# Optimization experiments

Measured on AMD Instinct MI355X. Metric: run time of the kernel, lower is better.

The kernel has to match this reference:

```python
import math
import jax, jax.numpy as jnp
import numpy as np

HEADS = 16
DIM_HEAD = 64
BSZ = 16        # block_size
EPS = 1e-8


def _flip_every_two(t):
    # t: (B, nblk, z, d) -> flip adjacent pairs along nblk
    B, nblk = t.shape[0], t.shape[1]
    t = t.reshape(B, nblk // 2, 2, *t.shape[2:])
    t = jnp.flip(t, axis=2)
    return t.reshape(B, nblk, *t.shape[3:])


def setup_inputs() -> dict:
    key = jax.random.key(0)
    k1, k2, k3 = jax.random.split(key, 3)
    b, n, dim = 4, 8192, 1024
    inner = HEADS * DIM_HEAD
    x = jax.random.normal(k1, (b, n, dim), dtype=jnp.float32)
    w_qkv = jax.random.normal(k2, (dim, inner * 3), dtype=jnp.float32) * 0.02
    w_out = jax.random.normal(k3, (inner, dim), dtype=jnp.float32) * 0.02
    b_out = jnp.zeros((dim,), dtype=jnp.float32)
    return {"x": x, "w_qkv": w_qkv, "w_out": w_out, "b_out": b_out}


def _hattention(x, w_qkv, w_out, b_out):
    b, n, dim = x.shape  # n assumed power of 2 -> no padding needed
    scale = DIM_HEAD ** -0.5

    qkv = x @ w_qkv                                   # (b, n, 3*inner)
    q, k, v = jnp.split(qkv, 3, axis=-1)

    def to_heads(t):
        return t.reshape(b, n, HEADS, DIM_HEAD).transpose(0, 2, 1, 3).reshape(b * HEADS, n, DIM_HEAD)

    q, k, v = map(to_heads, (q, k, v))
    q = q * scale

    num_levels = int(math.log2(n // BSZ)) - 1

    # build coarsened pyramid: q,k averaged over pairs, v summed
    qkvs = [(q, k, v)]
    for _ in range(num_levels):
        B, m, d = q.shape
        q = q.reshape(B, m // 2, 2, d).mean(axis=2)
        k = k.reshape(B, m // 2, 2, d).mean(axis=2)
        v = v.reshape(B, m // 2, 2, d).sum(axis=2)
        qkvs.append((q, k, v))

    def to_blocks(t):
        return t.reshape(t.shape[0], -1, BSZ, DIM_HEAD)

    Ys = []
    L = len(qkvs)
    for ind, (ql, kl, vl) in enumerate(reversed(qkvs)):
        is_last = ind == L - 1
        qb, kb, vb = map(to_blocks, (ql, kl, vl))
        if not is_last:
            kb = _flip_every_two(kb)
            vb = _flip_every_two(vb)
        # block-local unnormalized softmax attention
        S = jnp.einsum('bnid,bnjd->bnij', qb, kb)
        S = S - jnp.max(S, axis=-1, keepdims=True)
        A = jnp.exp(S)
        y = jnp.einsum('bnij,bnjd->bnid', A, vb)
        Asum = A.sum(axis=-1)
        Ys.append((y.reshape(y.shape[0], -1, DIM_HEAD),
                   Asum.reshape(Asum.shape[0], -1)))

    # combine coarse-to-fine by upsampling (repeat by 2) and summing
    Y, A = Ys[0]
    for Yl, Al in Ys[1:]:
        Y = jnp.repeat(Y, 2, axis=1) + Yl
        A = jnp.repeat(A, 2, axis=1) + Al

    out = Y / (A + EPS)[..., None]                    # (b*h, n, d)
    out = out.reshape(b, HEADS, n, DIM_HEAD).transpose(0, 2, 1, 3).reshape(b, n, HEADS * DIM_HEAD)
    return out @ w_out + b_out


def reference(x, w_qkv, w_out, b_out):
    return _hattention(x, w_qkv, w_out, b_out)
```

## Files before the change

### kernel.cpp

```cpp
#include <hip/hip_runtime.h>
#include <hip/hip_bf16.h>

typedef __bf16 bf16_t;
typedef bf16_t bf16x8 __attribute__((ext_vector_type(8)));
typedef float f32x4 __attribute__((ext_vector_type(4)));

#define PROWS 16352

__device__ __forceinline__ void gl_lds16(const bf16_t* g, bf16_t* l) {
  __builtin_amdgcn_global_load_lds(
      (const __attribute__((address_space(1))) void*)g,
      (__attribute__((address_space(3))) void*)l,
      16, 0, 0);
}

__device__ __forceinline__ void load8f(const bf16_t* p, float* f) {
  bf16x8 v = *(const bf16x8*)p;
#pragma unroll
  for (int e = 0; e < 8; ++e) f[e] = (float)v[e];
}
__device__ __forceinline__ void store8f(bf16_t* p, const float* f) {
  bf16x8 v;
#pragma unroll
  for (int e = 0; e < 8; ++e) v[e] = (bf16_t)f[e];
  *(bf16x8*)p = v;
}

__global__ __launch_bounds__(256) void cvt_f32_to_bf16(const float* __restrict__ in,
                                                       bf16_t* __restrict__ o) {
  size_t gid = (size_t)blockIdx.x * 256 + threadIdx.x;
  const float4* p = (const float4*)in + gid * 2;
  float4 a = p[0], b = p[1];
  bf16x8 v;
  v[0] = (bf16_t)a.x; v[1] = (bf16_t)a.y; v[2] = (bf16_t)a.z; v[3] = (bf16_t)a.w;
  v[4] = (bf16_t)b.x; v[5] = (bf16_t)b.y; v[6] = (bf16_t)b.z; v[7] = (bf16_t)b.w;
  *(bf16x8*)(o + gid * 8) = v;
}

__global__ __launch_bounds__(256) void transpose_to_bf16(const float* __restrict__ w,
                                                         bf16_t* __restrict__ wT,
                                                         int K, int N) {
  __shared__ float t[32][33];
  int bx = blockIdx.x, by = blockIdx.y;
  int tx = threadIdx.x & 31, ty = threadIdx.x >> 5;
#pragma unroll
  for (int r = ty; r < 32; r += 8)
    t[r][tx] = w[(size_t)(by * 32 + r) * N + bx * 32 + tx];
  __syncthreads();
#pragma unroll
  for (int r = ty; r < 32; r += 8)
    wT[(size_t)(bx * 32 + r) * K + by * 32 + tx] = (bf16_t)t[tx][r];
}

template <int EPI>
__global__ __launch_bounds__(512, 2) void gemm256(const bf16_t* __restrict__ A,
                                                  const bf16_t* __restrict__ Bt,
                                                  float* __restrict__ Cp,
                                                  const float* __restrict__ bias,
                                                  bf16_t* __restrict__ Pq,
                                                  bf16_t* __restrict__ Pk,
                                                  bf16_t* __restrict__ Pv,
                                                  int K, int ldc, int nTilesN) {
  __shared__ __align__(16) bf16_t As[2 * 256 * 64];
  __shared__ __align__(16) bf16_t Bs[2 * 256 * 64];
  const int tid = threadIdx.x;
  const int w = tid >> 6, lane = tid & 63;

  int mt, ntile;
  if (EPI == 0) {
    const int x = blockIdx.x & 7;
    const int c = blockIdx.x >> 3;
    mt = (x & 3) * 32 + c / 6;
    ntile = (x >> 2) * 6 + c % 6;
  } else {
    int nwg = gridDim.x;
    int chunk = nwg >> 3;
    int wgid = (blockIdx.x & 7) * chunk + (blockIdx.x >> 3);
    mt = wgid / nTilesN; ntile = wgid % nTilesN;
  }
  const int bm = mt * 256, bn = ntile * 256;

  const int wr = w >> 2, wc = w & 3;
  const int lr = lane & 15, lg = lane >> 4;
  const int sw = lr & 7;
  const int nt = K >> 6;

  f32x4 acc[8][4] = {};

  auto stageHalf = [&](const bf16_t* __restrict__ G, int rbase, int kt, int ld,
                       bf16_t* lbuf, int h) {
#pragma unroll
    for (int j = 0; j < 2; ++j) {
      int b = j * 8 + w;
      int r3 = lane >> 3;
      int k8 = (lane & 7) ^ r3;
      gl_lds16(G + (size_t)(rbase + h * 128 + b * 8 + r3) * ld + kt + k8 * 8,
               lbuf + h * 8192 + b * 512);
    }
  };

  stageHalf(Bt, bn, 0, K, Bs, 0); stageHalf(Bt, bn, 0, K, Bs, 1);
  stageHalf(A, bm, 0, K, As, 0);  stageHalf(A, bm, 0, K, As, 1);
  if (nt > 1) {
    stageHalf(Bt, bn, 64, K, Bs + 16384, 0); stageHalf(Bt, bn, 64, K, Bs + 16384, 1);
    stageHalf(A, bm, 64, K, As + 16384, 0);  stageHalf(A, bm, 64, K, As + 16384, 1);
    asm volatile("s_waitcnt vmcnt(8)" ::: "memory");
  } else {
    asm volatile("s_waitcnt vmcnt(0)" ::: "memory");
  }
  __syncthreads();

  for (int t = 0; t < nt; ++t) {
    const int c = t & 1;
    bf16_t* Abuf = As + c * 16384;
    bf16_t* Bbuf = Bs + c * 16384;
    const bool pf = (t + 2) < nt;
    const int kt2 = (t + 2) << 6;
    bf16x8 bfrag[4][2];

#pragma unroll
    for (int p = 0; p < 4; ++p) {
      bf16x8 afrag[2][2];
#pragma unroll
      for (int fi = 0; fi < 2; ++fi)
#pragma unroll
        for (int kk = 0; kk < 2; ++kk)
          afrag[fi][kk] = *(const bf16x8*)&Abuf[(wr * 128 + p * 32 + fi * 16 + lr) * 64 +
                                                (((kk * 4 + lg) ^ sw) * 8)];
      if (p == 0) {
#pragma unroll
        for (int fj = 0; fj < 4; ++fj)
#pragma unroll
          for (int kk = 0; kk < 2; ++kk)
            bfrag[fj][kk] = *(const bf16x8*)&Bbuf[(wc * 64 + fj * 16 + lr) * 64 +
                                                  (((kk * 4 + lg) ^ sw) * 8)];
      }
      if (pf) {
        if (p == 1) stageHalf(Bt, bn, kt2, K, Bbuf, 0);
        if (p == 2) stageHalf(Bt, bn, kt2, K, Bbuf, 1);
        if (p == 3) { stageHalf(A, bm, kt2, K, Abuf, 0); stageHalf(A, bm, kt2, K, Abuf, 1); }
      }
      __builtin_amdgcn_s_barrier();
      asm volatile("s_waitcnt lgkmcnt(0)" ::: "memory");
      __builtin_amdgcn_sched_barrier(0);
      __builtin_amdgcn_s_setprio(1);
#pragma unroll
      for (int kk = 0; kk < 2; ++kk)
#pragma unroll
        for (int fi = 0; fi < 2; ++fi)
#pragma unroll
          for (int fj = 0; fj < 4; ++fj)
            acc[p * 2 + fi][fj] = __builtin_amdgcn_mfma_f32_16x16x32_bf16(
                afrag[fi][kk], bfrag[fj][kk], acc[p * 2 + fi][fj], 0, 0, 0);
      __builtin_amdgcn_s_setprio(0);
      if (p == 3) {
        if (pf) asm volatile("s_waitcnt vmcnt(8)" ::: "memory");
        else    asm volatile("s_waitcnt vmcnt(0)" ::: "memory");
      }
      __builtin_amdgcn_s_barrier();
    }
  }

  if (EPI == 1) {
    float bv[4];
#pragma unroll
    for (int fj = 0; fj < 4; ++fj) bv[fj] = bias[bn + wc * 64 + fj * 16 + lr];
#pragma unroll
    for (int fi = 0; fi < 8; ++fi)
#pragma unroll
      for (int fj = 0; fj < 4; ++fj)
#pragma unroll
        for (int r = 0; r < 4; ++r) {
          int row = bm + wr * 128 + fi * 16 + lg * 4 + r;
          int col = bn + wc * 64 + fj * 16 + lr;
          Cp[(size_t)row * ldc + col] = acc[fi][fj][r] + bv[fj];
        }
  } else {
    const int tns = bn >> 10;
    const int h = ((bn & 1023) >> 6) + wc;
    const int hgRow = (bm >> 13) << 4;
    const int trow0 = (bm & 8191) + wr * 128;
    bf16_t* Pt = (tns == 0) ? Pq : (tns == 1 ? Pk : Pv);
    const float scl = (tns == 0) ? 0.125f : 1.f;
    bf16_t* lds = (w < 4) ? (As + w * 4608) : (Bs + (w - 4) * 4608);
    const size_t gbase = ((size_t)(hgRow + h) * PROWS + trow0) * 64;
#pragma unroll
    for (int half = 0; half < 2; ++half) {
#pragma unroll
      for (int fi4 = 0; fi4 < 4; ++fi4) {
        const int fi = half * 4 + fi4;
#pragma unroll
        for (int fj = 0; fj < 4; ++fj)
#pragma unroll
          for (int r = 0; r < 4; ++r)
            lds[(fi4 * 16 + lg * 4 + r) * 72 + fj * 16 + lr] =
                (bf16_t)(acc[fi][fj][r] * scl);
      }
      asm volatile("s_waitcnt lgkmcnt(0)" ::: "memory");
#pragma unroll
      for (int it = 0; it < 8; ++it) {
        const int row = it * 8 + (lane >> 3);
        bf16x8 v = *(const bf16x8*)&lds[row * 72 + (lane & 7) * 8];
        *(bf16x8*)(Pt + gbase + (size_t)(half * 64 + row) * 64 + (lane & 7) * 8) = v;
      }
      asm volatile("s_waitcnt lgkmcnt(0)" ::: "memory");
    }
  }
}

__global__ __launch_bounds__(256) void coarsen_lite(bf16_t* __restrict__ Pq,
                                                    bf16_t* __restrict__ Pk,
                                                    bf16_t* __restrict__ Pv) {
  __shared__ float l6s[4][64];
  const int poffA[9] = {0, 8192, 12288, 14336, 15360, 15872, 16128, 16256, 16320};
  const int hg = blockIdx.x >> 5, win = blockIdx.x & 31;
  const int tid = threadIdx.x;
  const int d8 = tid & 7, tb = tid >> 3, wv = tid >> 6;
  const size_t base = (size_t)hg * PROWS;
  const int r0 = win * 256 + tb * 8;

#pragma unroll 1
  for (int tensor = 0; tensor < 3; ++tensor) {
    bf16_t* P = (tensor == 0) ? Pq : (tensor == 1 ? Pk : Pv);
    const bool isv = (tensor == 2);
    float s3[8] = {}, t[8], o[8];
#pragma unroll
    for (int i = 0; i < 8; ++i) {
      load8f(P + (base + r0 + i) * 64 + d8 * 8, t);
#pragma unroll
      for (int e = 0; e < 8; ++e) s3[e] += t[e];
    }
    float s4[8], s5[8], s6[8];
#pragma unroll
    for (int e = 0; e < 8; ++e) s4[e] = s3[e] + __shfl_xor(s3[e], 8, 64);
    if ((tb & 1) == 0) {
      float sc = isv ? 1.f : 0.0625f;
#pragma unroll
      for (int e = 0; e < 8; ++e) o[e] = s4[e] * sc;
      store8f(P + (base + poffA[4] + win * 16 + (tb >> 1)) * 64 + d8 * 8, o);
    }
#pragma unroll
    for (int e = 0; e < 8; ++e) s5[e] = s4[e] + __shfl_xor(s4[e], 16, 64);
    if ((tb & 3) == 0) {
      float sc = isv ? 1.f : 0.03125f;
#pragma unroll
      for (int e = 0; e < 8; ++e) o[e] = s5[e] * sc;
      store8f(P + (base + poffA[5] + win * 8 + (tb >> 2)) * 64 + d8 * 8, o);
    }
#pragma unroll
    for (int e = 0; e < 8; ++e) s6[e] = s5[e] + __shfl_xor(s5[e], 32, 64);
    if ((tb & 7) == 0) {
      float sc = isv ? 1.f : 0.015625f;
#pragma unroll
      for (int e = 0; e < 8; ++e) { o[e] = s6[e] * sc; l6s[wv][d8 * 8 + e] = s6[e]; }
      store8f(P + (base + poffA[6] + win * 4 + wv) * 64 + d8 * 8, o);
    }
    __syncthreads();
    if (tid < 16) {
      int pr = tid >> 3, dd = tid & 7;
      float sc7 = isv ? 1.f : 0.0078125f;
#pragma unroll
      for (int e = 0; e < 8; ++e)
        o[e] = (l6s[2 * pr][dd * 8 + e] + l6s[2 * pr + 1][dd * 8 + e]) * sc7;
      store8f(P + (base + poffA[7] + win * 2 + pr) * 64 + dd * 8, o);
    }
    if (tid < 8) {
      float sc8 = isv ? 1.f : 0.00390625f;
#pragma unroll
      for (int e = 0; e < 8; ++e)
        o[e] = (l6s[0][d8 * 8 + e] + l6s[1][d8 * 8 + e] +
                l6s[2][d8 * 8 + e] + l6s[3][d8 * 8 + e]) * sc8;
      store8f(P + (base + poffA[8] + win) * 64 + d8 * 8, o);
    }
    __syncthreads();
  }
}

__global__ __launch_bounds__(256) void attn_hi(bf16_t* __restrict__ Pq,
                                               const bf16_t* __restrict__ Pk,
                                               const bf16_t* __restrict__ Pv,
                                               float* __restrict__ Asum) {
  const int poffA[9] = {0, 8192, 12288, 14336, 15360, 15872, 16128, 16256, 16320};
  const int tid = threadIdx.x;
  const int wv = tid >> 6, lane = tid & 63;
  const int lr = lane & 15, lg = lane >> 4;

  int bid = blockIdx.x * 4 + wv;
  int l = 4, cnt = 2048;
  while (bid >= cnt) { bid -= cnt; cnt >>= 1; ++l; }
  const int lg2nblk = 9 - l;
  const int blk = bid & ((1 << lg2nblk) - 1);
  const int hg = bid >> lg2nblk;
  const int kvblk = blk ^ 1;
  const size_t qbase = (size_t)hg * PROWS + poffA[l] + blk * 16;
  const size_t kvbase = (size_t)hg * PROWS + poffA[l] + kvblk * 16;

  f32x4 s = {};
#pragma unroll
  for (int c = 0; c < 2; ++c) {
    bf16x8 ak = *(const bf16x8*)(Pk + (kvbase + lr) * 64 + c * 32 + lg * 8);
    bf16x8 bq = *(const bf16x8*)(Pq + (qbase + lr) * 64 + c * 32 + lg * 8);
    s = __builtin_amdgcn_mfma_f32_16x16x32_bf16(ak, bq, s, 0, 0, 0);
  }
  float mx = fmaxf(fmaxf(s[0], s[1]), fmaxf(s[2], s[3]));
  mx = fmaxf(mx, __shfl_xor(mx, 16, 64));
  mx = fmaxf(mx, __shfl_xor(mx, 32, 64));
  float a[4]; float asum = 0.f;
#pragma unroll
  for (int r = 0; r < 4; ++r) { a[r] = (float)(bf16_t)__expf(s[r] - mx); asum += a[r]; }
  asum += __shfl_xor(asum, 16, 64);
  asum += __shfl_xor(asum, 32, 64);
  if (lg == 0) Asum[qbase + lr] = asum;

  const int src0 = (2 * lg) * 16 + lr;
  const int src1 = (2 * lg + 1) * 16 + lr;
  bf16x8 pa;
#pragma unroll
  for (int r = 0; r < 4; ++r) {
    float c0 = __shfl(a[r], src0, 64);
    float c1 = __shfl(a[r], src1, 64);
    pa[r]     = (lg < 2) ? (bf16_t)c0 : (bf16_t)0.f;
    pa[r + 4] = (lg < 2) ? (bf16_t)c1 : (bf16_t)0.f;
  }
#pragma unroll
  for (int dt = 0; dt < 4; ++dt) {
    bf16x8 vf;
    if (lg < 2) {
#pragma unroll
      for (int e = 0; e < 8; ++e) vf[e] = Pv[(kvbase + lg * 8 + e) * 64 + dt * 16 + lr];
    } else {
#pragma unroll
      for (int e = 0; e < 8; ++e) vf[e] = (bf16_t)0.f;
    }
    f32x4 y = __builtin_amdgcn_mfma_f32_16x16x32_bf16(pa, vf, (f32x4){}, 0, 0, 0);
#pragma unroll
    for (int r = 0; r < 4; ++r)
      Pq[(qbase + 4 * lg + r) * 64 + dt * 16 + lr] = (bf16_t)y[r];
  }
}

__global__ __launch_bounds__(256) void attn_comb(const bf16_t* __restrict__ Pq,
                                                 const bf16_t* __restrict__ Pk,
                                                 const bf16_t* __restrict__ Pv,
                                                 const float* __restrict__ Ab,
                                                 bf16_t* __restrict__ attnb) {
  __shared__ __align__(16) bf16_t yl[480 * 72];
  __shared__ float asl[480];
  const int poffA[9] = {0, 8192, 12288, 14336, 15360, 15872, 16128, 16256, 16320};
  const int loffA[4] = {0, 256, 384, 448};
  const int hg = blockIdx.x >> 5, win = blockIdx.x & 31;
  const int tid = threadIdx.x;
  const int wv = tid >> 6, lane = tid & 63;
  const int lr = lane & 15, lg = lane >> 4;
  const size_t hb = (size_t)hg * PROWS;

  auto do_attn = [&](int l, int blkL) {
    const int blk = win * (16 >> l) + blkL;
    const int kvblk = l ? (blk ^ 1) : blk;
    const int lrow = loffA[l] + blkL * 16;
    const int q0 = (blk * 16 + lr) << l;
    const int k0 = (kvblk * 16 + lr) << l;
    const int kv0 = (kvblk * 16) << l;
    const float scl = 1.f / (float)(1 << l);

    f32x4 s = {};
#pragma unroll
    for (int c = 0; c < 2; ++c) {
      float fk[8] = {}, fq[8] = {}, t[8];
      for (int m = 0; m < (1 << l); ++m) {
        load8f(Pk + (hb + k0 + m) * 64 + c * 32 + lg * 8, t);
#pragma unroll
        for (int e = 0; e < 8; ++e) fk[e] += t[e];
        load8f(Pq + (hb + q0 + m) * 64 + c * 32 + lg * 8, t);
#pragma unroll
        for (int e = 0; e < 8; ++e) fq[e] += t[e];
      }
      bf16x8 ak, bq;
#pragma unroll
      for (int e = 0; e < 8; ++e) {
        ak[e] = (bf16_t)(fk[e] * scl);
        bq[e] = (bf16_t)(fq[e] * scl);
      }
      s = __builtin_amdgcn_mfma_f32_16x16x32_bf16(ak, bq, s, 0, 0, 0);
    }

    float mx = fmaxf(fmaxf(s[0], s[1]), fmaxf(s[2], s[3]));
    mx = fmaxf(mx, __shfl_xor(mx, 16, 64));
    mx = fmaxf(mx, __shfl_xor(mx, 32, 64));
    float a[4]; float asum = 0.f;
#pragma unroll
    for (int r = 0; r < 4; ++r) { a[r] = (float)(bf16_t)__expf(s[r] - mx); asum += a[r]; }
    asum += __shfl_xor(asum, 16, 64);
    asum += __shfl_xor(asum, 32, 64);
    if (lg == 0) asl[lrow + lr] = asum;

    if (l == 0) {
      const int src0 = (2 * lg) * 16 + lr;
      const int src1 = (2 * lg + 1) * 16 + lr;
      bf16x8 pa;
#pragma unroll
      for (int r = 0; r < 4; ++r) {
        float c0 = __shfl(a[r], src0, 64);
        float c1 = __shfl(a[r], src1, 64);
        pa[r]     = (lg < 2) ? (bf16_t)c0 : (bf16_t)0.f;
        pa[r + 4] = (lg < 2) ? (bf16_t)c1 : (bf16_t)0.f;
      }
#pragma unroll
      for (int dt = 0; dt < 4; ++dt) {
        bf16x8 vf;
        if (lg < 2) {
#pragma unroll
          for (int e = 0; e < 8; ++e) vf[e] = Pv[(hb + kv0 + lg * 8 + e) * 64 + dt * 16 + lr];
        } else {
#pragma unroll
          for (int e = 0; e < 8; ++e) vf[e] = (bf16_t)0.f;
        }
        f32x4 y = __builtin_amdgcn_mfma_f32_16x16x32_bf16(pa, vf, (f32x4){}, 0, 0, 0);
#pragma unroll
        for (int r = 0; r < 4; ++r)
          yl[(lrow + 4 * lg + r) * 72 + dt * 16 + lr] = (bf16_t)y[r];
      }
    } else {
      const int nch = 1 << (l - 1);
      bf16x8 pa[4];
      for (int ch = 0; ch < nch; ++ch) {
        if (l == 1) {
#pragma unroll
          for (int e = 0; e < 8; ++e) pa[ch][e] = (bf16_t)a[e >> 1];
        } else if (l == 2) {
          int src = (2 * ch + (lg >> 1)) * 16 + lr;
          float t0 = __shfl(a[0], src, 64), t1 = __shfl(a[1], src, 64);
          float t2 = __shfl(a[2], src, 64), t3 = __shfl(a[3], src, 64);
          float vlo = (lg & 1) ? t2 : t0;
          float vhi = (lg & 1) ? t3 : t1;
#pragma unroll
          for (int e = 0; e < 4; ++e) { pa[ch][e] = (bf16_t)vlo; pa[ch][e + 4] = (bf16_t)vhi; }
        } else {
          int src = ch * 16 + lr;
          float t0 = __shfl(a[0], src, 64), t1 = __shfl(a[1], src, 64);
          float t2 = __shfl(a[2], src, 64), t3 = __shfl(a[3], src, 64);
          float v01 = (lg & 1) ? t1 : t0;
          float v23 = (lg & 1) ? t3 : t2;
          float vv = (lg & 2) ? v23 : v01;
#pragma unroll
          for (int e = 0; e < 8; ++e) pa[ch][e] = (bf16_t)vv;
        }
      }
#pragma unroll
      for (int dt = 0; dt < 4; ++dt) {
        f32x4 y = {};
        for (int ch = 0; ch < nch; ++ch) {
          bf16x8 vf;
#pragma unroll
          for (int e = 0; e < 8; ++e)
            vf[e] = Pv[(hb + kv0 + ch * 32 + lg * 8 + e) * 64 + dt * 16 + lr];
          y = __builtin_amdgcn_mfma_f32_16x16x32_bf16(pa[ch], vf, y, 0, 0, 0);
        }
#pragma unroll
        for (int r = 0; r < 4; ++r)
          yl[(lrow + 4 * lg + r) * 72 + dt * 16 + lr] = (bf16_t)y[r];
      }
    }
  };

  do_attn(0, wv * 4 + 0); do_attn(0, wv * 4 + 1);
  do_attn(0, wv * 4 + 2); do_attn(0, wv * 4 + 3);
  do_attn(1, wv * 2 + 0); do_attn(1, wv * 2 + 1);
  do_attn(2, wv);
  if (wv < 2) do_attn(3, wv);
  __syncthreads();

  const int d8 = tid & 7, rg = tid >> 3;
#pragma unroll
  for (int i = 0; i < 8; ++i) {
    const int r = rg * 8 + i;
    const int t = win * 256 + r;
    float acc[8] = {};
    float asum = 0.f;
#pragma unroll
    for (int l = 0; l < 4; ++l) {
      const int row = loffA[l] + (r >> l);
      asum += asl[row];
      bf16x8 v = *(const bf16x8*)&yl[row * 72 + d8 * 8];
#pragma unroll
      for (int e = 0; e < 8; ++e) acc[e] += (float)v[e];
    }
#pragma unroll
    for (int l = 4; l < 9; ++l) {
      const size_t grow = hb + poffA[l] + (t >> l);
      asum += Ab[grow];
      bf16x8 v = *(const bf16x8*)(Pq + grow * 64 + d8 * 8);
#pragma unroll
      for (int e = 0; e < 8; ++e) acc[e] += (float)v[e];
    }
    const float inv = 1.f / (asum + 1e-8f);
    bf16x8 o;
#pragma unroll
    for (int e = 0; e < 8; ++e) o[e] = (bf16_t)(acc[e] * inv);
    *(bf16x8*)(attnb + ((size_t)(hg >> 4) * 8192 + t) * 1024 + (hg & 15) * 64 + d8 * 8) = o;
  }
}

extern "C" void kernel_launch(void* const* d_in, const int* in_sizes, int n_in,
                              void* d_out, int out_size, void* d_ws, size_t ws_size,
                              hipStream_t stream) {
  const float* x = (const float*)d_in[0];
  const float* wqkv = (const float*)d_in[1];
  const float* wout = (const float*)d_in[2];
  const float* bout = (const float*)d_in[3];
  float* out = (float*)d_out;
  (void)in_sizes; (void)n_in; (void)out_size; (void)ws_size;

  char* base = (char*)d_ws;
  bf16_t* Pq    = (bf16_t*)(base + 0);
  bf16_t* Pk    = (bf16_t*)(base + 133955584);
  bf16_t* Pv    = (bf16_t*)(base + 267911168);
  float*  Ab    = (float*)(base + 401866752);
  bf16_t* woutT = (bf16_t*)(base + 406052864);
  bf16_t* x_bf  = (bf16_t*)(base + 408150016);
  bf16_t* wqkvT = (bf16_t*)(base + 475258880);
  bf16_t* attnb = (bf16_t*)(base + 408150016);

  cvt_f32_to_bf16<<<16384, 256, 0, stream>>>(x, x_bf);
  transpose_to_bf16<<<dim3(96, 32), 256, 0, stream>>>(wqkv, wqkvT, 1024, 3072);
  transpose_to_bf16<<<dim3(32, 32), 256, 0, stream>>>(wout, woutT, 1024, 1024);

  gemm256<0><<<1536, 512, 0, stream>>>(x_bf, wqkvT, nullptr, nullptr, Pq, Pk, Pv,
                                       1024, 3072, 12);

  coarsen_lite<<<2048, 256, 0, stream>>>(Pq, Pk, Pv);

  attn_hi<<<992, 256, 0, stream>>>(Pq, Pk, Pv, Ab);
  attn_comb<<<2048, 256, 0, stream>>>(Pq, Pk, Pv, Ab, attnb);

  gemm256<1><<<512, 512, 0, stream>>>(attnb, woutT, out, bout, nullptr, nullptr, nullptr,
                                      1024, 1024, 4);
}
```

Baseline: 541.3 us.

## Fuse coarse pyramid levels 4-8 into QKV GEMM epilogue, drop coarsen kernel

The QKV GEMM epilogue now reduces its accumulator tile across rows with wave shuffles and an LDS exchange between warps, and writes the pyramid levels 4 through 8 directly. The separate coarsen_lite kernel, which re-read the projected Q/K/V from global memory, is removed. This saves one launch and a full re-read of the level-0 data. In exchange the epilogue gains extra shuffles, scattered 2-byte global stores and two block-wide barriers.

```diff
diff --git a/kernel.cpp b/kernel.cpp
--- a/kernel.cpp
+++ b/kernel.cpp
@@ -18,12 +18,6 @@
   bf16x8 v = *(const bf16x8*)p;
 #pragma unroll
   for (int e = 0; e < 8; ++e) f[e] = (float)v[e];
-}
-__device__ __forceinline__ void store8f(bf16_t* p, const float* f) {
-  bf16x8 v;
-#pragma unroll
-  for (int e = 0; e < 8; ++e) v[e] = (bf16_t)f[e];
-  *(bf16x8*)p = v;
 }
 
 __global__ __launch_bounds__(256) void cvt_f32_to_bf16(const float* __restrict__ in,
@@ -182,8 +176,65 @@
     const int trow0 = (bm & 8191) + wr * 128;
     bf16_t* Pt = (tns == 0) ? Pq : (tns == 1 ? Pk : Pv);
     const float scl = (tns == 0) ? 0.125f : 1.f;
+    const size_t prow = (size_t)(hgRow + h) * PROWS;
+
+    {
+      const bool isv = (tns == 2);
+      const int tr = bm & 8191;
+      const int r4 = (tr >> 4) + wr * 8;
+      const int r5 = (tr >> 5) + wr * 4;
+      const int r6 = (tr >> 6) + wr * 2;
+      const int r7 = (tr >> 7) + wr;
+      const int r8 = (tr >> 8);
+      float* xch = (float*)(As + 20480) + w * 64;
+      float l7[4];
+#pragma unroll
+      for (int fj = 0; fj < 4; ++fj) {
+        const int col = fj * 16 + lr;
+        float rs[8];
+#pragma unroll
+        for (int g = 0; g < 8; ++g) {
+          float s = acc[g][fj][0] + acc[g][fj][1] + acc[g][fj][2] + acc[g][fj][3];
+          s += __shfl_xor(s, 16, 64);
+          s += __shfl_xor(s, 32, 64);
+          rs[g] = s;
+        }
+        l7[fj] = (rs[0] + rs[1] + rs[2] + rs[3]) + (rs[4] + rs[5] + rs[6] + rs[7]);
+        if (lg == 0) {
+          const float m4 = isv ? 1.f : scl * 0.0625f;
+          const float m5 = isv ? 1.f : scl * 0.03125f;
+          const float m6 = isv ? 1.f : scl * 0.015625f;
+          const float m7 = isv ? 1.f : scl * 0.0078125f;
+#pragma unroll
+          for (int g = 0; g < 8; ++g)
+            Pt[(prow + 15360 + r4 + g) * 64 + col] = (bf16_t)(rs[g] * m4);
+#pragma unroll
+          for (int g = 0; g < 4; ++g)
+            Pt[(prow + 15872 + r5 + g) * 64 + col] =
+                (bf16_t)((rs[2 * g] + rs[2 * g + 1]) * m5);
+#pragma unroll
+          for (int g = 0; g < 2; ++g)
+            Pt[(prow + 16128 + r6 + g) * 64 + col] =
+                (bf16_t)(((rs[4 * g] + rs[4 * g + 1]) + (rs[4 * g + 2] + rs[4 * g + 3])) * m6);
+          Pt[(prow + 16256 + r7) * 64 + col] = (bf16_t)(l7[fj] * m7);
+          xch[col] = l7[fj];
+        }
+      }
+      __syncthreads();
+      if (wr == 0 && lg == 0) {
+        const float m8 = isv ? 1.f : scl * 0.00390625f;
+        const float* pxch = (const float*)(As + 20480) + (w + 4) * 64;
+#pragma unroll
+        for (int fj = 0; fj < 4; ++fj) {
+          const int col = fj * 16 + lr;
+          Pt[(prow + 16320 + r8) * 64 + col] = (bf16_t)((l7[fj] + pxch[col]) * m8);
+        }
+      }
+      __syncthreads();
+    }
+
     bf16_t* lds = (w < 4) ? (As + w * 4608) : (Bs + (w - 4) * 4608);
-    const size_t gbase = ((size_t)(hgRow + h) * PROWS + trow0) * 64;
+    const size_t gbase = (prow + trow0) * 64;
 #pragma unroll
     for (int half = 0; half < 2; ++half) {
 #pragma unroll
@@ -205,74 +256,6 @@
       }
       asm volatile("s_waitcnt lgkmcnt(0)" ::: "memory");
     }
-  }
-}
-
-__global__ __launch_bounds__(256) void coarsen_lite(bf16_t* __restrict__ Pq,
-                                                    bf16_t* __restrict__ Pk,
-                                                    bf16_t* __restrict__ Pv) {
-  __shared__ float l6s[4][64];
-  const int poffA[9] = {0, 8192, 12288, 14336, 15360, 15872, 16128, 16256, 16320};
-  const int hg = blockIdx.x >> 5, win = blockIdx.x & 31;
-  const int tid = threadIdx.x;
-  const int d8 = tid & 7, tb = tid >> 3, wv = tid >> 6;
-  const size_t base = (size_t)hg * PROWS;
-  const int r0 = win * 256 + tb * 8;
-
-#pragma unroll 1
-  for (int tensor = 0; tensor < 3; ++tensor) {
-    bf16_t* P = (tensor == 0) ? Pq : (tensor == 1 ? Pk : Pv);
-    const bool isv = (tensor == 2);
-    float s3[8] = {}, t[8], o[8];
-#pragma unroll
-    for (int i = 0; i < 8; ++i) {
-      load8f(P + (base + r0 + i) * 64 + d8 * 8, t);
-#pragma unroll
-      for (int e = 0; e < 8; ++e) s3[e] += t[e];
-    }
-    float s4[8], s5[8], s6[8];
-#pragma unroll
-    for (int e = 0; e < 8; ++e) s4[e] = s3[e] + __shfl_xor(s3[e], 8, 64);
-    if ((tb & 1) == 0) {
-      float sc = isv ? 1.f : 0.0625f;
-#pragma unroll
-      for (int e = 0; e < 8; ++e) o[e] = s4[e] * sc;
-      store8f(P + (base + poffA[4] + win * 16 + (tb >> 1)) * 64 + d8 * 8, o);
-    }
-#pragma unroll
-    for (int e = 0; e < 8; ++e) s5[e] = s4[e] + __shfl_xor(s4[e], 16, 64);
-    if ((tb & 3) == 0) {
-      float sc = isv ? 1.f : 0.03125f;
-#pragma unroll
-      for (int e = 0; e < 8; ++e) o[e] = s5[e] * sc;
-      store8f(P + (base + poffA[5] + win * 8 + (tb >> 2)) * 64 + d8 * 8, o);
-    }
-#pragma unroll
-    for (int e = 0; e < 8; ++e) s6[e] = s5[e] + __shfl_xor(s5[e], 32, 64);
-    if ((tb & 7) == 0) {
-      float sc = isv ? 1.f : 0.015625f;
-#pragma unroll
-      for (int e = 0; e < 8; ++e) { o[e] = s6[e] * sc; l6s[wv][d8 * 8 + e] = s6[e]; }
-      store8f(P + (base + poffA[6] + win * 4 + wv) * 64 + d8 * 8, o);
-    }
-    __syncthreads();
-    if (tid < 16) {
-      int pr = tid >> 3, dd = tid & 7;
-      float sc7 = isv ? 1.f : 0.0078125f;
-#pragma unroll
-      for (int e = 0; e < 8; ++e)
-        o[e] = (l6s[2 * pr][dd * 8 + e] + l6s[2 * pr + 1][dd * 8 + e]) * sc7;
-      store8f(P + (base + poffA[7] + win * 2 + pr) * 64 + dd * 8, o);
-    }
-    if (tid < 8) {
-      float sc8 = isv ? 1.f : 0.00390625f;
-#pragma unroll
-      for (int e = 0; e < 8; ++e)
-        o[e] = (l6s[0][d8 * 8 + e] + l6s[1][d8 * 8 + e] +
-                l6s[2][d8 * 8 + e] + l6s[3][d8 * 8 + e]) * sc8;
-      store8f(P + (base + poffA[8] + win) * 64 + d8 * 8, o);
-    }
-    __syncthreads();
   }
 }
 
@@ -528,8 +511,6 @@
   gemm256<0><<<1536, 512, 0, stream>>>(x_bf, wqkvT, nullptr, nullptr, Pq, Pk, Pv,
                                        1024, 3072, 12);
 
-  coarsen_lite<<<2048, 256, 0, stream>>>(Pq, Pk, Pv);
-
   attn_hi<<<992, 256, 0, stream>>>(Pq, Pk, Pv, Ab);
   attn_comb<<<2048, 256, 0, stream>>>(Pq, Pk, Pv, Ab, attnb);
 
```

New measurement: 514.1 us. 1.05x faster.
